# Kernel optimization log

Hardware: AMD Instinct MI355X
Metric: run time of the kernel (lower is better)

Reference implementation:

```python
import jax, jax.numpy as jnp
import numpy as np

CODEBOOK_SIZE = 1024
EMBEDDING_DIM = 64


def setup_inputs() -> dict:
    key = jax.random.key(0)
    k_in, k_cb = jax.random.split(key)
    # latent feature (batch, embedding_dim, length)
    input = jax.random.normal(k_in, (16, EMBEDDING_DIM, 8192), dtype=jnp.float32)
    # learned codebook table (codebook_size, embedding_dim)
    codebook = jax.random.normal(k_cb, (CODEBOOK_SIZE, EMBEDDING_DIM), dtype=jnp.float32)
    return {"input": input, "codebook": codebook}


def reference(input, codebook):
    # input: (B, D, T); codebook: (K, D)
    B, D = input.shape[0], input.shape[1]
    spatial = input.shape[2:]
    # move embedding dim last and flatten tokens: (B*T, D)
    x = jnp.moveaxis(input, 1, -1).reshape(-1, D)
    x_sq = jnp.sum(x * x, axis=-1, keepdims=True)            # (N, 1)
    e_sq = jnp.sum(codebook * codebook, axis=-1)             # (K,)
    dist = x_sq - 2.0 * (x @ codebook.T) + e_sq[None, :]     # (N, K)
    indices = jnp.argmin(dist, axis=-1)                      # (N,)
    quantized = jnp.take(codebook, indices, axis=0)          # (N, D)
    # reshape back: output (B, D, *spatial), indices (B, *spatial)
    out = jnp.moveaxis(quantized.reshape((B,) + spatial + (D,)), -1, 1)
    idx = indices.reshape((B,) + spatial)
    return out, idx
```

## Files before the change

kernel.cpp:

```cpp
#include <hip/hip_runtime.h>
#include <float.h>

#define K_CODES 1024
#define DIM 64
#define T_LEN 8192
#define N_TOK 131072
#define LO_SCALE 2048.0f

typedef _Float16 half8 __attribute__((ext_vector_type(8)));
typedef float    f32x4 __attribute__((ext_vector_type(4)));

#define MFMA16(a, b, c) __builtin_amdgcn_mfma_f32_16x16x32_f16((a), (b), (c), 0, 0, 0)

__global__ void vq_prep(const float* __restrict__ cb,
                        _Float16* __restrict__ w,
                        float* __restrict__ wesq) {
    __shared__ float part[128];
    const int ct   = blockIdx.x;
    const int r    = threadIdx.x;
    const int halF = r >> 7;
    const int rr   = r & 127;
    const int q    = rr >> 4;
    const int code = rr & 15;

    const float* src = cb + (size_t)(ct * 16 + code) * DIM + q * 8;
    float4 v0 = *reinterpret_cast<const float4*>(src);
    float4 v1 = *reinterpret_cast<const float4*>(src + 4);
    float x[8] = {v0.x, v0.y, v0.z, v0.w, v1.x, v1.y, v1.z, v1.w};

    half8 o;
    float psum = 0.0f;
    #pragma unroll
    for (int j = 0; j < 8; ++j) {
        _Float16 h = (_Float16)x[j];
        o[j] = halF ? (_Float16)((x[j] - (float)h) * LO_SCALE) : h;
        psum = fmaf(x[j], x[j], psum);
    }
    *reinterpret_cast<half8*>(w + (size_t)ct * 2048 + halF * 1024 + q * 128 + code * 8) = o;

    if (halF == 0) part[rr] = psum;
    __syncthreads();
    if (r < 16) {
        float s = 0.0f;
        #pragma unroll
        for (int q2 = 0; q2 < 8; ++q2) s += part[q2 * 16 + r];
        wesq[ct * 16 + r] = s * LO_SCALE;
    }
}

__global__ __launch_bounds__(256, 2)
void vq_main(const float* __restrict__ in,
             const float* __restrict__ cb,
             const _Float16* __restrict__ w,
             const float* __restrict__ wesq,
             float* __restrict__ out) {
    __shared__ float esq_s[K_CODES];
    __shared__ int   idx_s[256];

    const int tid  = threadIdx.x;
    const int wave = tid >> 6;
    const int lane = tid & 63;
    const int lo4  = lane & 15;
    const int quad = lane >> 4;

    for (int k = tid; k < K_CODES; k += 256) esq_s[k] = wesq[k];
    __syncthreads();

    const int strip = blockIdx.x * 256 + wave * 64;
    const int b  = strip >> 13;
    const int t0 = strip & 8191;

    const float* xin = in + (size_t)b * DIM * T_LEN + t0;
    half8 a_h[4][2], a_hs[4][2], a_l[4][2];
    #pragma unroll
    for (int mt = 0; mt < 4; ++mt) {
        #pragma unroll
        for (int s = 0; s < 2; ++s) {
            half8 hh, hs, ll;
            #pragma unroll
            for (int j = 0; j < 8; ++j) {
                const int d = s * 32 + quad * 8 + j;
                float xv = -2.0f * xin[(size_t)d * T_LEN + mt * 16 + lo4];
                _Float16 h = (_Float16)xv;
                hh[j] = h;
                hs[j] = (_Float16)((float)h * LO_SCALE);
                ll[j] = (_Float16)((xv - (float)h) * LO_SCALE);
            }
            a_h[mt][s] = hh;
            a_hs[mt][s] = hs;
            a_l[mt][s] = ll;
        }
    }

    float best[16];
    int   bidx[16];
    #pragma unroll
    for (int i = 0; i < 16; ++i) { best[i] = FLT_MAX; bidx[i] = 0; }

    const _Float16* wb = w + (size_t)lane * 8;

    half8 Ah0, Ah1, Al0, Al1, Bh0, Bh1, Bl0, Bl1;
    float Ae, Be;
    auto loadB = [&](int ct, half8& h0, half8& h1, half8& l0, half8& l1, float& es) {
        const _Float16* p = wb + (size_t)ct * 2048;
        h0 = *reinterpret_cast<const half8*>(p);
        h1 = *reinterpret_cast<const half8*>(p + 512);
        l0 = *reinterpret_cast<const half8*>(p + 1024);
        l1 = *reinterpret_cast<const half8*>(p + 1536);
        es = esq_s[ct * 16 + lo4];
    };
    auto step = [&](const half8& h0, const half8& h1, const half8& l0,
                    const half8& l1, float es, int ct) {
        const int code = ct * 16 + lo4;
        #pragma unroll
        for (int mt = 0; mt < 4; ++mt) {
            f32x4 c = {es, es, es, es};
            c = MFMA16(a_hs[mt][0], h0, c);
            c = MFMA16(a_hs[mt][1], h1, c);
            c = MFMA16(a_h[mt][0], l0, c);
            c = MFMA16(a_h[mt][1], l1, c);
            c = MFMA16(a_l[mt][0], h0, c);
            c = MFMA16(a_l[mt][1], h1, c);
            #pragma unroll
            for (int r = 0; r < 4; ++r) {
                float sc = c[r];
                const int i = mt * 4 + r;
                bool lt = sc < best[i];
                best[i] = lt ? sc : best[i];
                bidx[i] = lt ? code : bidx[i];
            }
        }
    };

    loadB(0, Ah0, Ah1, Al0, Al1, Ae);
    loadB(1, Bh0, Bh1, Bl0, Bl1, Be);
    for (int p = 0; p < 31; ++p) {
        step(Ah0, Ah1, Al0, Al1, Ae, 2 * p);
        loadB(2 * p + 2, Ah0, Ah1, Al0, Al1, Ae);
        step(Bh0, Bh1, Bl0, Bl1, Be, 2 * p + 1);
        loadB(2 * p + 3, Bh0, Bh1, Bl0, Bl1, Be);
    }
    step(Ah0, Ah1, Al0, Al1, Ae, 62);
    step(Bh0, Bh1, Bl0, Bl1, Be, 63);

    #pragma unroll
    for (int i = 0; i < 16; ++i) {
        float s = best[i];
        int  ix = bidx[i];
        #pragma unroll
        for (int off = 1; off < 16; off <<= 1) {
            float s2 = __shfl_xor(s, off, 64);
            int  ix2 = __shfl_xor(ix, off, 64);
            bool take = (s2 < s) || (s2 == s && ix2 < ix);
            s  = take ? s2 : s;
            ix = take ? ix2 : ix;
        }
        if (lo4 == 0) {
            idx_s[wave * 64 + (i >> 2) * 16 + quad * 4 + (i & 3)] = ix;
        }
    }
    __syncthreads();

    const int token = blockIdx.x * 256 + tid;
    const int tb = token >> 13;
    const int tt = token & 8191;
    const int my_idx = idx_s[tid];

    out[(size_t)N_TOK * DIM + token] = (float)my_idx;

    const float* crow = cb + (size_t)my_idx * DIM;
    float* outv = out + (size_t)tb * DIM * T_LEN + tt;
    #pragma unroll
    for (int d0 = 0; d0 < DIM; d0 += 4) {
        float4 v = *reinterpret_cast<const float4*>(crow + d0);
        outv[(size_t)(d0 + 0) * T_LEN] = v.x;
        outv[(size_t)(d0 + 1) * T_LEN] = v.y;
        outv[(size_t)(d0 + 2) * T_LEN] = v.z;
        outv[(size_t)(d0 + 3) * T_LEN] = v.w;
    }
}

extern "C" void kernel_launch(void* const* d_in, const int* in_sizes, int n_in,
                              void* d_out, int out_size, void* d_ws, size_t ws_size,
                              hipStream_t stream) {
    const float* in = (const float*)d_in[0];
    const float* cb = (const float*)d_in[1];
    float* out = (float*)d_out;

    _Float16* w   = (_Float16*)d_ws;
    float*   wesq = (float*)((char*)d_ws + 64 * 4096);

    vq_prep<<<dim3(64), dim3(256), 0, stream>>>(cb, w, wesq);
    vq_main<<<dim3(N_TOK / 256), dim3(256), 0, stream>>>(in, cb, w, wesq, out);
}
```

Measured before the change: 129.0 us.

## Stage most of the split-half codebook in LDS with 512-thread blocks

Doubles the block size to 512 threads (8 waves) and copies the first 36 code tiles of the preprocessed fp16 codebook into dynamic shared memory at block start. The inner loop then reads those tiles from LDS and only the remaining tiles from global/L2. The goal is less global-memory traffic per wave, since all eight waves share the staged tiles. In exchange there is a large up-front copy per block, a branch in the load path, and about 154 KB of LDS per block, which limits blocks per CU.

```diff
diff --git a/kernel.cpp b/kernel.cpp
--- a/kernel.cpp
+++ b/kernel.cpp
@@ -6,6 +6,8 @@
 #define T_LEN 8192
 #define N_TOK 131072
 #define LO_SCALE 2048.0f
+#define NT_LDS 36
+#define LDS_BYTES (NT_LDS * 4096 + 4096 + 2048)
 
 typedef _Float16 half8 __attribute__((ext_vector_type(8)));
 typedef float    f32x4 __attribute__((ext_vector_type(4)));
@@ -48,14 +50,16 @@
     }
 }
 
-__global__ __launch_bounds__(256, 2)
+__global__ __launch_bounds__(512, 2)
 void vq_main(const float* __restrict__ in,
              const float* __restrict__ cb,
              const _Float16* __restrict__ w,
              const float* __restrict__ wesq,
              float* __restrict__ out) {
-    __shared__ float esq_s[K_CODES];
-    __shared__ int   idx_s[256];
+    extern __shared__ __align__(16) char smem[];
+    _Float16* wlds  = (_Float16*)smem;
+    float*    esq_s = (float*)(smem + NT_LDS * 4096);
+    int*      idx_s = (int*)(smem + NT_LDS * 4096 + 4096);
 
     const int tid  = threadIdx.x;
     const int wave = tid >> 6;
@@ -63,10 +67,18 @@
     const int lo4  = lane & 15;
     const int quad = lane >> 4;
 
-    for (int k = tid; k < K_CODES; k += 256) esq_s[k] = wesq[k];
+    {
+        const float4* gs = (const float4*)w;
+        float4*       ls = (float4*)wlds;
+        #pragma unroll 6
+        for (int i = 0; i < NT_LDS * 4096 / 16 / 512; ++i)
+            ls[i * 512 + tid] = gs[i * 512 + tid];
+        #pragma unroll
+        for (int k = tid; k < K_CODES; k += 512) esq_s[k] = wesq[k];
+    }
     __syncthreads();
 
-    const int strip = blockIdx.x * 256 + wave * 64;
+    const int strip = blockIdx.x * 512 + wave * 64;
     const int b  = strip >> 13;
     const int t0 = strip & 8191;
 
@@ -97,16 +109,25 @@
     #pragma unroll
     for (int i = 0; i < 16; ++i) { best[i] = FLT_MAX; bidx[i] = 0; }
 
-    const _Float16* wb = w + (size_t)lane * 8;
+    const _Float16* wb_g = w    + (size_t)lane * 8;
+    const _Float16* wb_l = wlds + (size_t)lane * 8;
 
     half8 Ah0, Ah1, Al0, Al1, Bh0, Bh1, Bl0, Bl1;
     float Ae, Be;
     auto loadB = [&](int ct, half8& h0, half8& h1, half8& l0, half8& l1, float& es) {
-        const _Float16* p = wb + (size_t)ct * 2048;
-        h0 = *reinterpret_cast<const half8*>(p);
-        h1 = *reinterpret_cast<const half8*>(p + 512);
-        l0 = *reinterpret_cast<const half8*>(p + 1024);
-        l1 = *reinterpret_cast<const half8*>(p + 1536);
+        if (ct < NT_LDS) {
+            const _Float16* p = wb_l + (size_t)ct * 2048;
+            h0 = *reinterpret_cast<const half8*>(p);
+            h1 = *reinterpret_cast<const half8*>(p + 512);
+            l0 = *reinterpret_cast<const half8*>(p + 1024);
+            l1 = *reinterpret_cast<const half8*>(p + 1536);
+        } else {
+            const _Float16* p = wb_g + (size_t)ct * 2048;
+            h0 = *reinterpret_cast<const half8*>(p);
+            h1 = *reinterpret_cast<const half8*>(p + 512);
+            l0 = *reinterpret_cast<const half8*>(p + 1024);
+            l1 = *reinterpret_cast<const half8*>(p + 1536);
+        }
         es = esq_s[ct * 16 + lo4];
     };
     auto step = [&](const half8& h0, const half8& h1, const half8& l0,
@@ -161,7 +182,7 @@
     }
     __syncthreads();
 
-    const int token = blockIdx.x * 256 + tid;
+    const int token = blockIdx.x * 512 + tid;
     const int tb = token >> 13;
     const int tt = token & 8191;
     const int my_idx = idx_s[tid];
@@ -190,6 +211,13 @@
     _Float16* w   = (_Float16*)d_ws;
     float*   wesq = (float*)((char*)d_ws + 64 * 4096);
 
+    static bool attr_done = false;
+    if (!attr_done) {
+        hipFuncSetAttribute(reinterpret_cast<const void*>(vq_main),
+                            hipFuncAttributeMaxDynamicSharedMemorySize, LDS_BYTES);
+        attr_done = true;
+    }
+
     vq_prep<<<dim3(64), dim3(256), 0, stream>>>(cb, w, wesq);
-    vq_main<<<dim3(N_TOK / 256), dim3(256), 0, stream>>>(in, cb, w, wesq, out);
+    vq_main<<<dim3(N_TOK / 512), dim3(512), LDS_BYTES, stream>>>(in, cb, w, wesq, out);
 }
```

New measurement: 132.9 us. +3.0%, slower.

## Use single fp16 MFMA pass with error-bound margin and exact fallback rescoring

Applied to the files above, without the earlier changes.

Replaces the three-term split-precision (hi/lo) MFMA distance computation with a single hi-only fp16 pass, cutting MFMA work per tile to a third and halving codebook loads. It tracks the best and second-best score per token and computes a per-token error bound from the norms of the dropped low parts plus a slack constant. Tokens whose gap falls inside that margin are queued and rescored exactly in double precision against the full codebook staged through shared memory. The risk is that a large queue makes the slow fallback dominate, and the added shared memory (doubles, ebuf, esq4) may reduce occupancy.

```diff
diff --git a/kernel.cpp b/kernel.cpp
--- a/kernel.cpp
+++ b/kernel.cpp
@@ -1,11 +1,13 @@
 #include <hip/hip_runtime.h>
 #include <float.h>
+#include <math.h>
 
 #define K_CODES 1024
 #define DIM 64
 #define T_LEN 8192
 #define N_TOK 131072
 #define LO_SCALE 2048.0f
+#define SLOP 24.0f
 
 typedef _Float16 half8 __attribute__((ext_vector_type(8)));
 typedef float    f32x4 __attribute__((ext_vector_type(4)));
@@ -14,8 +16,10 @@
 
 __global__ void vq_prep(const float* __restrict__ cb,
                         _Float16* __restrict__ w,
-                        float* __restrict__ wesq) {
-    __shared__ float part[128];
+                        float* __restrict__ wesq,
+                        float* __restrict__ wbh2,
+                        float* __restrict__ wbl2) {
+    __shared__ float part_x[128], part_h[128], part_l[128];
     const int ct   = blockIdx.x;
     const int r    = threadIdx.x;
     const int halF = r >> 7;
@@ -29,22 +33,36 @@
     float x[8] = {v0.x, v0.y, v0.z, v0.w, v1.x, v1.y, v1.z, v1.w};
 
     half8 o;
-    float psum = 0.0f;
+    float psx = 0.0f, psq = 0.0f;
     #pragma unroll
     for (int j = 0; j < 8; ++j) {
         _Float16 h = (_Float16)x[j];
-        o[j] = halF ? (_Float16)((x[j] - (float)h) * LO_SCALE) : h;
-        psum = fmaf(x[j], x[j], psum);
+        if (halF) {
+            _Float16 lv = (_Float16)((x[j] - (float)h) * LO_SCALE);
+            o[j] = lv;
+            psq = fmaf((float)lv, (float)lv, psq);
+        } else {
+            o[j] = h;
+            psq = fmaf((float)h, (float)h, psq);
+            psx = fmaf(x[j], x[j], psx);
+        }
     }
     *reinterpret_cast<half8*>(w + (size_t)ct * 2048 + halF * 1024 + q * 128 + code * 8) = o;
 
-    if (halF == 0) part[rr] = psum;
+    if (halF == 0) { part_x[rr] = psx; part_h[rr] = psq; }
+    else           { part_l[rr] = psq; }
     __syncthreads();
     if (r < 16) {
-        float s = 0.0f;
-        #pragma unroll
-        for (int q2 = 0; q2 < 8; ++q2) s += part[q2 * 16 + r];
-        wesq[ct * 16 + r] = s * LO_SCALE;
+        float sx = 0.0f, sh = 0.0f, sl = 0.0f;
+        #pragma unroll
+        for (int q2 = 0; q2 < 8; ++q2) {
+            sx += part_x[q2 * 16 + r];
+            sh += part_h[q2 * 16 + r];
+            sl += part_l[q2 * 16 + r];
+        }
+        wesq[ct * 16 + r] = sx * LO_SCALE;
+        wbh2[ct * 16 + r] = sh;
+        wbl2[ct * 16 + r] = sl;
     }
 }
 
@@ -53,9 +71,17 @@
              const float* __restrict__ cb,
              const _Float16* __restrict__ w,
              const float* __restrict__ wesq,
+             const float* __restrict__ wbh2,
+             const float* __restrict__ wbl2,
              float* __restrict__ out) {
-    __shared__ float esq_s[K_CODES];
-    __shared__ int   idx_s[256];
+    __shared__ __align__(16) float esq4[K_CODES][4];
+    __shared__ int    idx_s[256];
+    __shared__ int    queue[256];
+    __shared__ int    qn;
+    __shared__ float  wmx[8];
+    __shared__ float  ebuf[64][65];
+    __shared__ double fbest[256];
+    __shared__ int    fidx[256];
 
     const int tid  = threadIdx.x;
     const int wave = tid >> 6;
@@ -63,103 +89,179 @@
     const int lo4  = lane & 15;
     const int quad = lane >> 4;
 
-    for (int k = tid; k < K_CODES; k += 256) esq_s[k] = wesq[k];
+    float pmh = 0.0f, pml = 0.0f;
+    for (int k = tid; k < K_CODES; k += 256) {
+        float e = wesq[k];
+        float4 ev = {e, e, e, e};
+        *reinterpret_cast<float4*>(&esq4[k][0]) = ev;
+        pmh = fmaxf(pmh, wbh2[k]);
+        pml = fmaxf(pml, wbl2[k]);
+    }
+    #pragma unroll
+    for (int off = 1; off < 64; off <<= 1) {
+        pmh = fmaxf(pmh, __shfl_xor(pmh, off, 64));
+        pml = fmaxf(pml, __shfl_xor(pml, off, 64));
+    }
+    if (lane == 0) { wmx[wave] = pmh; wmx[4 + wave] = pml; }
+    if (tid == 0) qn = 0;
     __syncthreads();
+    const float BH = sqrtf(fmaxf(fmaxf(wmx[0], wmx[1]), fmaxf(wmx[2], wmx[3])));
+    const float BL = sqrtf(fmaxf(fmaxf(wmx[4], wmx[5]), fmaxf(wmx[6], wmx[7])));
 
     const int strip = blockIdx.x * 256 + wave * 64;
     const int b  = strip >> 13;
     const int t0 = strip & 8191;
 
     const float* xin = in + (size_t)b * DIM * T_LEN + t0;
-    half8 a_h[4][2], a_hs[4][2], a_l[4][2];
+    half8 a_hs[4][2];
+    float marg[4];
     #pragma unroll
     for (int mt = 0; mt < 4; ++mt) {
+        float nh = 0.0f, nl = 0.0f;
         #pragma unroll
         for (int s = 0; s < 2; ++s) {
-            half8 hh, hs, ll;
+            half8 hs;
             #pragma unroll
             for (int j = 0; j < 8; ++j) {
                 const int d = s * 32 + quad * 8 + j;
                 float xv = -2.0f * xin[(size_t)d * T_LEN + mt * 16 + lo4];
                 _Float16 h = (_Float16)xv;
-                hh[j] = h;
-                hs[j] = (_Float16)((float)h * LO_SCALE);
-                ll[j] = (_Float16)((xv - (float)h) * LO_SCALE);
-            }
-            a_h[mt][s] = hh;
+                float hf = (float)h;
+                hs[j] = (_Float16)(hf * LO_SCALE);
+                _Float16 lv = (_Float16)((xv - hf) * LO_SCALE);
+                float lf = (float)lv;
+                nh = fmaf(hf, hf, nh);
+                nl = fmaf(lf, lf, nl);
+            }
             a_hs[mt][s] = hs;
-            a_l[mt][s] = ll;
-        }
-    }
-
-    float best[16];
-    int   bidx[16];
-    #pragma unroll
-    for (int i = 0; i < 16; ++i) { best[i] = FLT_MAX; bidx[i] = 0; }
+        }
+        nh += __shfl_xor(nh, 16, 64);  nh += __shfl_xor(nh, 32, 64);
+        nl += __shfl_xor(nl, 16, 64);  nl += __shfl_xor(nl, 32, 64);
+        marg[mt] = sqrtf(nh) * BL + sqrtf(nl) * BH + SLOP;
+    }
+
+    float b1[16], b2[16];
+    int   i1[16];
+    #pragma unroll
+    for (int i = 0; i < 16; ++i) { b1[i] = FLT_MAX; b2[i] = FLT_MAX; i1[i] = 0; }
 
     const _Float16* wb = w + (size_t)lane * 8;
 
-    half8 Ah0, Ah1, Al0, Al1, Bh0, Bh1, Bl0, Bl1;
-    float Ae, Be;
-    auto loadB = [&](int ct, half8& h0, half8& h1, half8& l0, half8& l1, float& es) {
+    auto step = [&](const half8& h0, const half8& h1, int ct) {
+        const int code = ct * 16 + lo4;
+        f32x4 ci = *reinterpret_cast<const f32x4*>(&esq4[code][0]);
+        f32x4 c0 = MFMA16(a_hs[0][0], h0, ci);
+        f32x4 c1 = MFMA16(a_hs[1][0], h0, ci);
+        f32x4 c2 = MFMA16(a_hs[2][0], h0, ci);
+        f32x4 c3 = MFMA16(a_hs[3][0], h0, ci);
+        c0 = MFMA16(a_hs[0][1], h1, c0);
+        c1 = MFMA16(a_hs[1][1], h1, c1);
+        c2 = MFMA16(a_hs[2][1], h1, c2);
+        c3 = MFMA16(a_hs[3][1], h1, c3);
+        f32x4 cc[4] = {c0, c1, c2, c3};
+        #pragma unroll
+        for (int mt = 0; mt < 4; ++mt) {
+            #pragma unroll
+            for (int r = 0; r < 4; ++r) {
+                float sc = cc[mt][r];
+                const int i = mt * 4 + r;
+                bool lt = sc < b1[i];
+                float mn2 = fminf(b2[i], sc);
+                b2[i] = lt ? b1[i] : mn2;
+                b1[i] = lt ? sc : b1[i];
+                i1[i] = lt ? code : i1[i];
+            }
+        }
+    };
+    auto loadH = [&](int ct, half8& h0, half8& h1) {
         const _Float16* p = wb + (size_t)ct * 2048;
         h0 = *reinterpret_cast<const half8*>(p);
         h1 = *reinterpret_cast<const half8*>(p + 512);
-        l0 = *reinterpret_cast<const half8*>(p + 1024);
-        l1 = *reinterpret_cast<const half8*>(p + 1536);
-        es = esq_s[ct * 16 + lo4];
     };
-    auto step = [&](const half8& h0, const half8& h1, const half8& l0,
-                    const half8& l1, float es, int ct) {
-        const int code = ct * 16 + lo4;
-        #pragma unroll
-        for (int mt = 0; mt < 4; ++mt) {
-            f32x4 c = {es, es, es, es};
-            c = MFMA16(a_hs[mt][0], h0, c);
-            c = MFMA16(a_hs[mt][1], h1, c);
-            c = MFMA16(a_h[mt][0], l0, c);
-            c = MFMA16(a_h[mt][1], l1, c);
-            c = MFMA16(a_l[mt][0], h0, c);
-            c = MFMA16(a_l[mt][1], h1, c);
-            #pragma unroll
-            for (int r = 0; r < 4; ++r) {
-                float sc = c[r];
-                const int i = mt * 4 + r;
-                bool lt = sc < best[i];
-                best[i] = lt ? sc : best[i];
-                bidx[i] = lt ? code : bidx[i];
-            }
-        }
-    };
-
-    loadB(0, Ah0, Ah1, Al0, Al1, Ae);
-    loadB(1, Bh0, Bh1, Bl0, Bl1, Be);
+
+    half8 A0, A1, B0, B1;
+    loadH(0, A0, A1);
+    loadH(1, B0, B1);
     for (int p = 0; p < 31; ++p) {
-        step(Ah0, Ah1, Al0, Al1, Ae, 2 * p);
-        loadB(2 * p + 2, Ah0, Ah1, Al0, Al1, Ae);
-        step(Bh0, Bh1, Bl0, Bl1, Be, 2 * p + 1);
-        loadB(2 * p + 3, Bh0, Bh1, Bl0, Bl1, Be);
-    }
-    step(Ah0, Ah1, Al0, Al1, Ae, 62);
-    step(Bh0, Bh1, Bl0, Bl1, Be, 63);
+        step(A0, A1, 2 * p);     loadH(2 * p + 2, A0, A1);
+        step(B0, B1, 2 * p + 1); loadH(2 * p + 3, B0, B1);
+    }
+    step(A0, A1, 62);
+    step(B0, B1, 63);
 
     #pragma unroll
     for (int i = 0; i < 16; ++i) {
-        float s = best[i];
-        int  ix = bidx[i];
+        float s = b1[i], s2 = b2[i];
+        int ix = i1[i];
         #pragma unroll
         for (int off = 1; off < 16; off <<= 1) {
-            float s2 = __shfl_xor(s, off, 64);
-            int  ix2 = __shfl_xor(ix, off, 64);
-            bool take = (s2 < s) || (s2 == s && ix2 < ix);
-            s  = take ? s2 : s;
-            ix = take ? ix2 : ix;
-        }
+            float os  = __shfl_xor(s,  off, 64);
+            float os2 = __shfl_xor(s2, off, 64);
+            int  oix  = __shfl_xor(ix, off, 64);
+            float mx = fmaxf(s, os);
+            s2 = fminf(fminf(s2, os2), mx);
+            bool take = (os < s) || (os == s && oix < ix);
+            s  = take ? os  : s;
+            ix = take ? oix : ix;
+        }
+        float mtok = __shfl(marg[i >> 2], quad * 16 + quad * 4 + (i & 3), 64);
         if (lo4 == 0) {
-            idx_s[wave * 64 + (i >> 2) * 16 + quad * 4 + (i & 3)] = ix;
+            int tl = wave * 64 + (i >> 2) * 16 + quad * 4 + (i & 3);
+            idx_s[tl] = ix;
+            if (!(s2 - s > 2.0f * mtok)) {
+                int slot = atomicAdd(&qn, 1);
+                queue[slot] = tl;
+            }
         }
     }
     __syncthreads();
+
+    const int nq = qn;
+    if (nq > 0) {
+        fbest[tid] = 1e300;
+        fidx[tid]  = 0;
+        for (int ch = 0; ch < 16; ++ch) {
+            __syncthreads();
+            {
+                int row = tid >> 2, c0 = (tid & 3) * 16;
+                const float* srcp = cb + (size_t)(ch * 64 + row) * DIM + c0;
+                #pragma unroll
+                for (int jj = 0; jj < 16; ++jj) ebuf[row][c0 + jj] = srcp[jj];
+            }
+            __syncthreads();
+            for (int qi = wave; qi < nq; qi += 4) {
+                int tl = queue[qi];
+                int g  = blockIdx.x * 256 + tl;
+                int gb = g >> 13, gt = g & 8191;
+                float xl = in[(size_t)gb * DIM * T_LEN + (size_t)lane * T_LEN + gt];
+                double dsum = 0.0;
+                const int mycode = ch * 64 + lane;
+                for (int d = 0; d < 64; ++d) {
+                    float xd = __shfl(xl, d, 64);
+                    float ed = ebuf[lane][d];
+                    double df = (double)xd - (double)ed;
+                    dsum = fma(df, df, dsum);
+                }
+                double s = dsum; int ix = mycode;
+                #pragma unroll
+                for (int off = 1; off < 64; off <<= 1) {
+                    double os = __shfl_xor(s, off, 64);
+                    int   oix = __shfl_xor(ix, off, 64);
+                    bool take = (os < s) || (os == s && oix < ix);
+                    s  = take ? os  : s;
+                    ix = take ? oix : ix;
+                }
+                if (lane == 0) {
+                    if (s < fbest[tl] || (s == fbest[tl] && ix < fidx[tl])) {
+                        fbest[tl] = s; fidx[tl] = ix;
+                    }
+                }
+            }
+        }
+        __syncthreads();
+        if (tid < nq) { int tl = queue[tid]; idx_s[tl] = fidx[tl]; }
+        __syncthreads();
+    }
 
     const int token = blockIdx.x * 256 + tid;
     const int tb = token >> 13;
@@ -188,8 +290,10 @@
     float* out = (float*)d_out;
 
     _Float16* w   = (_Float16*)d_ws;
-    float*   wesq = (float*)((char*)d_ws + 64 * 4096);
-
-    vq_prep<<<dim3(64), dim3(256), 0, stream>>>(cb, w, wesq);
-    vq_main<<<dim3(N_TOK / 256), dim3(256), 0, stream>>>(in, cb, w, wesq, out);
+    float* wesq = (float*)((char*)d_ws + 64 * 4096);
+    float* wbh2 = (float*)((char*)d_ws + 64 * 4096 + 4096);
+    float* wbl2 = (float*)((char*)d_ws + 64 * 4096 + 8192);
+
+    vq_prep<<<dim3(64), dim3(256), 0, stream>>>(cb, w, wesq, wbh2, wbl2);
+    vq_main<<<dim3(N_TOK / 256), dim3(256), 0, stream>>>(in, cb, w, wesq, wbh2, wbl2, out);
 }
```

Result: slower. 302.2 us (+134.3%).

## Software-pipeline MFMA chains with argmin and stagger wave start

Applied to the files above, without the earlier changes.

The MFMA sequence is reordered to interleave four independent accumulator chains, so dependent MFMAs no longer stall back-to-back. The argmin compare for one code tile is deferred so it overlaps the MFMAs of the next tile, with two sets of accumulators alternating. The first codebook tile loads are hoisted ahead of the input conversion, and waves are staggered with s_sleep so they do not all contend for the matrix unit in phase. This raises register pressure from the extra accumulators and adds a small startup delay.

```diff
diff --git a/kernel.cpp b/kernel.cpp
--- a/kernel.cpp
+++ b/kernel.cpp
@@ -66,9 +66,32 @@
     for (int k = tid; k < K_CODES; k += 256) esq_s[k] = wesq[k];
     __syncthreads();
 
+    {
+        const int ph = ((blockIdx.x & 1) << 1) | (wave & 1);
+        if (ph == 1)      __builtin_amdgcn_s_sleep(4);
+        else if (ph == 2) __builtin_amdgcn_s_sleep(8);
+        else if (ph == 3) __builtin_amdgcn_s_sleep(12);
+    }
+
     const int strip = blockIdx.x * 256 + wave * 64;
     const int b  = strip >> 13;
     const int t0 = strip & 8191;
+
+    const _Float16* wb = w + (size_t)lane * 8;
+
+    half8 Ah0, Ah1, Al0, Al1, Bh0, Bh1, Bl0, Bl1;
+    float Ae, Be;
+    auto loadB = [&](int ct, half8& h0, half8& h1, half8& l0, half8& l1, float& es) {
+        const _Float16* p = wb + (size_t)ct * 2048;
+        h0 = *reinterpret_cast<const half8*>(p);
+        h1 = *reinterpret_cast<const half8*>(p + 512);
+        l0 = *reinterpret_cast<const half8*>(p + 1024);
+        l1 = *reinterpret_cast<const half8*>(p + 1536);
+        es = esq_s[ct * 16 + lo4];
+    };
+
+    loadB(0, Ah0, Ah1, Al0, Al1, Ae);
+    loadB(1, Bh0, Bh1, Bl0, Bl1, Be);
 
     const float* xin = in + (size_t)b * DIM * T_LEN + t0;
     half8 a_h[4][2], a_hs[4][2], a_l[4][2];
@@ -97,33 +120,44 @@
     #pragma unroll
     for (int i = 0; i < 16; ++i) { best[i] = FLT_MAX; bidx[i] = 0; }
 
-    const _Float16* wb = w + (size_t)lane * 8;
-
-    half8 Ah0, Ah1, Al0, Al1, Bh0, Bh1, Bl0, Bl1;
-    float Ae, Be;
-    auto loadB = [&](int ct, half8& h0, half8& h1, half8& l0, half8& l1, float& es) {
-        const _Float16* p = wb + (size_t)ct * 2048;
-        h0 = *reinterpret_cast<const half8*>(p);
-        h1 = *reinterpret_cast<const half8*>(p + 512);
-        l0 = *reinterpret_cast<const half8*>(p + 1024);
-        l1 = *reinterpret_cast<const half8*>(p + 1536);
-        es = esq_s[ct * 16 + lo4];
+    auto mstep = [&](const half8& h0, const half8& h1, const half8& l0,
+                     const half8& l1, float es,
+                     f32x4& o0, f32x4& o1, f32x4& o2, f32x4& o3) {
+        f32x4 ci = {es, es, es, es};
+        o0 = MFMA16(a_hs[0][0], h0, ci);
+        o1 = MFMA16(a_hs[1][0], h0, ci);
+        o2 = MFMA16(a_hs[2][0], h0, ci);
+        o3 = MFMA16(a_hs[3][0], h0, ci);
+        o0 = MFMA16(a_hs[0][1], h1, o0);
+        o1 = MFMA16(a_hs[1][1], h1, o1);
+        o2 = MFMA16(a_hs[2][1], h1, o2);
+        o3 = MFMA16(a_hs[3][1], h1, o3);
+        o0 = MFMA16(a_h[0][0], l0, o0);
+        o1 = MFMA16(a_h[1][0], l0, o1);
+        o2 = MFMA16(a_h[2][0], l0, o2);
+        o3 = MFMA16(a_h[3][0], l0, o3);
+        o0 = MFMA16(a_h[0][1], l1, o0);
+        o1 = MFMA16(a_h[1][1], l1, o1);
+        o2 = MFMA16(a_h[2][1], l1, o2);
+        o3 = MFMA16(a_h[3][1], l1, o3);
+        o0 = MFMA16(a_l[0][0], h0, o0);
+        o1 = MFMA16(a_l[1][0], h0, o1);
+        o2 = MFMA16(a_l[2][0], h0, o2);
+        o3 = MFMA16(a_l[3][0], h0, o3);
+        o0 = MFMA16(a_l[0][1], h1, o0);
+        o1 = MFMA16(a_l[1][1], h1, o1);
+        o2 = MFMA16(a_l[2][1], h1, o2);
+        o3 = MFMA16(a_l[3][1], h1, o3);
     };
-    auto step = [&](const half8& h0, const half8& h1, const half8& l0,
-                    const half8& l1, float es, int ct) {
+    auto amin = [&](const f32x4& c0, const f32x4& c1, const f32x4& c2,
+                    const f32x4& c3, int ct) {
         const int code = ct * 16 + lo4;
+        f32x4 cc[4] = {c0, c1, c2, c3};
         #pragma unroll
         for (int mt = 0; mt < 4; ++mt) {
-            f32x4 c = {es, es, es, es};
-            c = MFMA16(a_hs[mt][0], h0, c);
-            c = MFMA16(a_hs[mt][1], h1, c);
-            c = MFMA16(a_h[mt][0], l0, c);
-            c = MFMA16(a_h[mt][1], l1, c);
-            c = MFMA16(a_l[mt][0], h0, c);
-            c = MFMA16(a_l[mt][1], h1, c);
             #pragma unroll
             for (int r = 0; r < 4; ++r) {
-                float sc = c[r];
+                float sc = cc[mt][r];
                 const int i = mt * 4 + r;
                 bool lt = sc < best[i];
                 best[i] = lt ? sc : best[i];
@@ -132,16 +166,26 @@
         }
     };
 
-    loadB(0, Ah0, Ah1, Al0, Al1, Ae);
-    loadB(1, Bh0, Bh1, Bl0, Bl1, Be);
-    for (int p = 0; p < 31; ++p) {
-        step(Ah0, Ah1, Al0, Al1, Ae, 2 * p);
+    f32x4 x0, x1, x2, x3, y0, y1, y2, y3;
+
+    mstep(Ah0, Ah1, Al0, Al1, Ae, x0, x1, x2, x3);
+    loadB(2, Ah0, Ah1, Al0, Al1, Ae);
+    mstep(Bh0, Bh1, Bl0, Bl1, Be, y0, y1, y2, y3);
+    amin(x0, x1, x2, x3, 0);
+    loadB(3, Bh0, Bh1, Bl0, Bl1, Be);
+    for (int p = 1; p <= 30; ++p) {
+        mstep(Ah0, Ah1, Al0, Al1, Ae, x0, x1, x2, x3);
+        amin(y0, y1, y2, y3, 2 * p - 1);
         loadB(2 * p + 2, Ah0, Ah1, Al0, Al1, Ae);
-        step(Bh0, Bh1, Bl0, Bl1, Be, 2 * p + 1);
+        mstep(Bh0, Bh1, Bl0, Bl1, Be, y0, y1, y2, y3);
+        amin(x0, x1, x2, x3, 2 * p);
         loadB(2 * p + 3, Bh0, Bh1, Bl0, Bl1, Be);
     }
-    step(Ah0, Ah1, Al0, Al1, Ae, 62);
-    step(Bh0, Bh1, Bl0, Bl1, Be, 63);
+    mstep(Ah0, Ah1, Al0, Al1, Ae, x0, x1, x2, x3);
+    amin(y0, y1, y2, y3, 61);
+    mstep(Bh0, Bh1, Bl0, Bl1, Be, y0, y1, y2, y3);
+    amin(x0, x1, x2, x3, 62);
+    amin(y0, y1, y2, y3, 63);
 
     #pragma unroll
     for (int i = 0; i < 16; ++i) {
```

Measured after the change: 130.1 us. No clear change (+0.9%).
